# Kernel optimization log

Measured on AMD Instinct MI355X. Metric: run time of the kernel, lower is better.

Reference implementation:

```python
import jax, jax.numpy as jnp
import numpy as np

VOCAB, D, H = 32000, 256, 1024
B, S = 8, 4096
PAD = 0


def setup_inputs() -> dict:
    key = jax.random.key(0)
    ks = jax.random.split(key, 9)
    x = jax.random.randint(ks[0], (B, S), 0, VOCAB)
    emb = jax.random.normal(ks[1], (VOCAB, D), jnp.float32) * 0.02
    wq = jax.random.normal(ks[2], (D, D), jnp.float32) * 0.02
    wk = jax.random.normal(ks[3], (D, D), jnp.float32) * 0.02
    wv = jax.random.normal(ks[4], (D, D), jnp.float32) * 0.02
    w1 = jax.random.normal(ks[5], (H, D), jnp.float32) * 0.02
    b1 = jnp.zeros((H,), jnp.float32)
    w2 = jax.random.normal(ks[6], (VOCAB, H), jnp.float32) * 0.02
    b2 = jnp.zeros((VOCAB,), jnp.float32)
    return {"x": x, "emb": emb, "wq": wq, "wk": wk, "wv": wv,
            "w1": w1, "b1": b1, "w2": w2, "b2": b2}


def reference(x, emb, wq, wk, wv, w1, b1, w2, b2):
    # padding_idx=0: that embedding row is zero
    emb0 = emb.at[PAD].set(0.0)
    e = emb0[x]                                   # [B,S,D]
    keep = (x != PAD).astype(e.dtype)             # 1 where key is NOT masked
    q = jnp.einsum('bsd,ed->bse', e, wq)
    k = jnp.einsum('bsd,ed->bse', e, wk)
    v = jnp.einsum('bsd,ed->bse', e, wv)
    # Original: attn = q @ k^T, masked_fill padded keys -> 0, v_out = (attn @ v).sum(dim=1)
    # Reordered (identical math, O(S*D^2) instead of O(S^2)):
    #   v_out[b,:] = (sum_i q_i) @ (sum_j keep_j * k_j v_j^T)
    qsum = q.sum(axis=1)                          # [B,D]
    kv = jnp.einsum('bsd,bse->bde', k * keep[..., None], v)  # [B,D,D]
    v_out = jnp.einsum('bd,bde->be', qsum, kv)    # [B,D]
    h = jax.nn.relu(v_out @ w1.T + b1)            # [B,H]
    logits = h @ w2.T + b2                        # [B,VOCAB]
    return jax.nn.softmax(logits, axis=-1)
```

## Files before the change

kernel.cpp:

```cpp
#include <hip/hip_runtime.h>

#define BB 8
#define SS 4096
#define DD 256
#define HH 1024
#define VOCAB 32000
#define NCH 128
#define NLB 2000

typedef float v2f __attribute__((ext_vector_type(2)));


__global__ __launch_bounds__(256) void k_esum(const int* __restrict__ x,
        const float* __restrict__ emb, float* __restrict__ part_esum) {
    __shared__ int toks[32];
    const int b = blockIdx.y, chunk = blockIdx.x, tid = threadIdx.x;
    if (tid < 32) toks[tid] = x[b * SS + chunk * 32 + tid];
    __syncthreads();
    float a0 = 0.f, a1 = 0.f, a2 = 0.f, a3 = 0.f;
    for (int t = 0; t < 32; t += 4) {
        int t0 = toks[t], t1 = toks[t + 1], t2 = toks[t + 2], t3 = toks[t + 3];
        if (t0) a0 += emb[t0 * DD + tid];
        if (t1) a1 += emb[t1 * DD + tid];
        if (t2) a2 += emb[t2 * DD + tid];
        if (t3) a3 += emb[t3 * DD + tid];
    }
    part_esum[(b * NCH + chunk) * DD + tid] = (a0 + a1) + (a2 + a3);
}

__global__ __launch_bounds__(256) void k_qa(const float* __restrict__ part_esum,
        const float* __restrict__ wq, const float* __restrict__ wk,
        float* __restrict__ a) {
    const int b = blockIdx.x, tid = threadIdx.x, wid = tid >> 6, lane = tid & 63;
    __shared__ __align__(16) float es[DD];
    __shared__ __align__(16) float qs[DD];
    {
        float s0 = 0.f, s1 = 0.f, s2 = 0.f, s3 = 0.f;
        const float* p = part_esum + b * NCH * DD + tid;
        for (int c = 0; c < NCH; c += 4) {
            s0 += p[(c + 0) * DD]; s1 += p[(c + 1) * DD];
            s2 += p[(c + 2) * DD]; s3 += p[(c + 3) * DD];
        }
        es[tid] = (s0 + s1) + (s2 + s3);
    }
    __syncthreads();
    const float4 es4 = ((const float4*)es)[lane];
    for (int r0 = 0; r0 < 64; r0 += 4) {
        float dp[4];
        #pragma unroll
        for (int j = 0; j < 4; ++j) {
            const float4 w4 = ((const float4*)(wq + (wid * 64 + r0 + j) * DD))[lane];
            dp[j] = w4.x * es4.x + w4.y * es4.y + w4.z * es4.z + w4.w * es4.w;
        }
        #pragma unroll
        for (int off = 32; off; off >>= 1) {
            #pragma unroll
            for (int j = 0; j < 4; ++j) dp[j] += __shfl_xor(dp[j], off, 64);
        }
        if (lane < 4) qs[wid * 64 + r0 + lane] = dp[lane];
    }
    __syncthreads();
    float a0 = 0.f, a1 = 0.f, a2 = 0.f, a3 = 0.f;
    for (int e = 0; e < DD; e += 4) {
        a0 += wk[(e + 0) * DD + tid] * qs[e + 0];
        a1 += wk[(e + 1) * DD + tid] * qs[e + 1];
        a2 += wk[(e + 2) * DD + tid] * qs[e + 2];
        a3 += wk[(e + 3) * DD + tid] * qs[e + 3];
    }
    a[b * DD + tid] = (a0 + a1) + (a2 + a3);
}

__global__ __launch_bounds__(256) void k_u(const int* __restrict__ x,
        const float* __restrict__ emb, const float* __restrict__ a,
        float* __restrict__ part_u) {
    const int b = blockIdx.y, chunk = blockIdx.x, tid = threadIdx.x;
    const int wid = tid >> 6, lane = tid & 63;
    __shared__ int toks[32];
    __shared__ __align__(16) float ured[4][DD];
    if (tid < 32) toks[tid] = x[b * SS + chunk * 32 + tid];
    __syncthreads();
    const float4 a4 = ((const float4*)(a + b * DD))[lane];
    float4 up = {0.f, 0.f, 0.f, 0.f};
    #pragma unroll
    for (int tt = 0; tt < 32; tt += 16) {
        int tok[4]; float4 e4[4]; float dp[4];
        #pragma unroll
        for (int j = 0; j < 4; ++j) tok[j] = toks[tt + j * 4 + wid];
        #pragma unroll
        for (int j = 0; j < 4; ++j) {
            e4[j] = ((const float4*)(emb + tok[j] * DD))[lane];
            dp[j] = e4[j].x * a4.x + e4[j].y * a4.y + e4[j].z * a4.z + e4[j].w * a4.w;
        }
        #pragma unroll
        for (int off = 32; off; off >>= 1) {
            #pragma unroll
            for (int j = 0; j < 4; ++j) dp[j] += __shfl_xor(dp[j], off, 64);
        }
        #pragma unroll
        for (int j = 0; j < 4; ++j) {
            const float m = (tok[j] != 0) ? dp[j] : 0.f;
            up.x += m * e4[j].x; up.y += m * e4[j].y;
            up.z += m * e4[j].z; up.w += m * e4[j].w;
        }
    }
    ((float4*)ured[wid])[lane] = up;
    __syncthreads();
    part_u[(b * NCH + chunk) * DD + tid] =
        ured[0][tid] + ured[1][tid] + ured[2][tid] + ured[3][tid];
}

__global__ __launch_bounds__(256) void k_vout(const float* __restrict__ part_u,
        const float* __restrict__ wv, float* __restrict__ vout) {
    const int b = blockIdx.x, tid = threadIdx.x, wid = tid >> 6, lane = tid & 63;
    __shared__ __align__(16) float us[DD];
    {
        float s0 = 0.f, s1 = 0.f, s2 = 0.f, s3 = 0.f;
        const float* p = part_u + b * NCH * DD + tid;
        for (int c = 0; c < NCH; c += 4) {
            s0 += p[(c + 0) * DD]; s1 += p[(c + 1) * DD];
            s2 += p[(c + 2) * DD]; s3 += p[(c + 3) * DD];
        }
        us[tid] = (s0 + s1) + (s2 + s3);
    }
    __syncthreads();
    const float4 u4 = ((const float4*)us)[lane];
    for (int r0 = 0; r0 < 64; r0 += 4) {
        float dp[4];
        #pragma unroll
        for (int j = 0; j < 4; ++j) {
            const float4 w4 = ((const float4*)(wv + (wid * 64 + r0 + j) * DD))[lane];
            dp[j] = w4.x * u4.x + w4.y * u4.y + w4.z * u4.z + w4.w * u4.w;
        }
        #pragma unroll
        for (int off = 32; off; off >>= 1) {
            #pragma unroll
            for (int j = 0; j < 4; ++j) dp[j] += __shfl_xor(dp[j], off, 64);
        }
        if (lane < 4) vout[b * DD + wid * 64 + r0 + lane] = dp[lane];
    }
}

__global__ __launch_bounds__(256) void k_h(const float* __restrict__ vout,
        const float* __restrict__ w1, const float* __restrict__ b1,
        float* __restrict__ h) {
    const int b = blockIdx.y, tid = threadIdx.x, wid = tid >> 6, lane = tid & 63;
    const float4 v4 = ((const float4*)(vout + b * DD))[lane];
    const int rbase = blockIdx.x * 32 + wid * 8;
    float dp[8];
    #pragma unroll
    for (int r = 0; r < 8; ++r) {
        const float4 w4 = ((const float4*)(w1 + (rbase + r) * DD))[lane];
        dp[r] = w4.x * v4.x + w4.y * v4.y + w4.z * v4.z + w4.w * v4.w;
    }
    #pragma unroll
    for (int off = 32; off; off >>= 1) {
        #pragma unroll
        for (int r = 0; r < 8; ++r) dp[r] += __shfl_xor(dp[r], off, 64);
    }
    if (lane < 8) h[b * HH + rbase + lane] = fmaxf(dp[lane] + b1[rbase + lane], 0.f);
}

__global__ __launch_bounds__(256, 4) void k_logits(const float* __restrict__ h,
        const float* __restrict__ w2, const float* __restrict__ b2,
        float* __restrict__ out, float* __restrict__ spart) {
    const int tid = threadIdx.x, wid = tid >> 6, lane = tid & 63;
    const int half = lane >> 5;
    v2f hp[16];
    #pragma unroll
    for (int c = 0; c < 4; ++c) {
        const float4 ta = ((const float4*)(h + (2 * wid)     * HH + c * 256))[lane];
        const float4 tb = ((const float4*)(h + (2 * wid + 1) * HH + c * 256))[lane];
        hp[c * 4 + 0] = (v2f){ta.x, tb.x};
        hp[c * 4 + 1] = (v2f){ta.y, tb.y};
        hp[c * 4 + 2] = (v2f){ta.z, tb.z};
        hp[c * 4 + 3] = (v2f){ta.w, tb.w};
    }
    float m_run = -1e30f, s_run = 0.f;
    #pragma unroll 2
    for (int r = 0; r < 16; ++r) {
        const int i = blockIdx.x + r * NLB;
        const float4* row = (const float4*)(w2 + (size_t)i * HH);
        v2f acc = (v2f){0.f, 0.f};
        #pragma unroll
        for (int c = 0; c < 4; ++c) {
            const float4 w = row[c * 64 + lane];
            acc += hp[c * 4 + 0] * w.x;
            acc += hp[c * 4 + 1] * w.y;
            acc += hp[c * 4 + 2] * w.z;
            acc += hp[c * 4 + 3] * w.w;
        }
        const float send = (half == 0) ? acc.y : acc.x;
        const float keep = (half == 0) ? acc.x : acc.y;
        float s = keep + __shfl_xor(send, 32, 64);
        s += __shfl_xor(s, 16, 64);
        s += __shfl_xor(s, 8, 64);
        s += __shfl_xor(s, 4, 64);
        s += __shfl_xor(s, 2, 64);
        s += __shfl_xor(s, 1, 64);
        if ((lane & 31) == 0) {
            const float lg = s + b2[i];
            out[(2 * wid + half) * VOCAB + i] = lg;
            const float mn = fmaxf(m_run, lg);
            s_run = s_run * __expf(m_run - mn) + __expf(lg - mn);
            m_run = mn;
        }
    }
    if ((lane & 31) == 0)
        ((v2f*)spart)[(2 * wid + half) * NLB + blockIdx.x] = (v2f){m_run, s_run};
}

__global__ __launch_bounds__(256) void k_norm(const float* __restrict__ spart,
        float* __restrict__ out) {
    const int b = blockIdx.y, seg = blockIdx.x, tid = threadIdx.x;
    __shared__ float rm[256], rs[256];
    const v2f* p = (const v2f*)spart + b * NLB;
    float m = -1e30f, s = 0.f;
    for (int idx = tid; idx < NLB; idx += 256) {
        const v2f t = p[idx];
        const float mn = fmaxf(m, t.x);
        s = s * __expf(m - mn) + t.y * __expf(t.x - mn);
        m = mn;
    }
    rm[tid] = m; rs[tid] = s;
    __syncthreads();
    for (int st = 128; st; st >>= 1) {
        if (tid < st) {
            const float m2 = rm[tid + st], s2 = rs[tid + st];
            const float mn = fmaxf(rm[tid], m2);
            rs[tid] = rs[tid] * __expf(rm[tid] - mn) + s2 * __expf(m2 - mn);
            rm[tid] = mn;
        }
        __syncthreads();
    }
    const float gm = rm[0], ginv = 1.f / rs[0];
    float* lg = out + b * VOCAB + seg * 2000;
    for (int i = tid; i < 2000; i += 256) lg[i] = __expf(lg[i] - gm) * ginv;
}

extern "C" void kernel_launch(void* const* d_in, const int* in_sizes, int n_in,
                              void* d_out, int out_size, void* d_ws, size_t ws_size,
                              hipStream_t stream) {
    const int*   x   = (const int*)d_in[0];
    const float* emb = (const float*)d_in[1];
    const float* wq  = (const float*)d_in[2];
    const float* wk  = (const float*)d_in[3];
    const float* wv  = (const float*)d_in[4];
    const float* w1  = (const float*)d_in[5];
    const float* b1  = (const float*)d_in[6];
    const float* w2  = (const float*)d_in[7];
    const float* b2  = (const float*)d_in[8];
    float* out = (float*)d_out;
    float* ws  = (float*)d_ws;

    float* part_esum = ws;
    float* part_u    = ws + 262144;
    float* a         = ws + 524288;
    float* vout      = ws + 526336;
    float* h         = ws + 528384;
    float* spart     = ws + 536576;

    k_esum<<<dim3(NCH, BB), 256, 0, stream>>>(x, emb, part_esum);
    k_qa<<<BB, 256, 0, stream>>>(part_esum, wq, wk, a);
    k_u<<<dim3(NCH, BB), 256, 0, stream>>>(x, emb, a, part_u);
    k_vout<<<BB, 256, 0, stream>>>(part_u, wv, vout);
    k_h<<<dim3(32, BB), 256, 0, stream>>>(vout, w1, b1, h);
    k_logits<<<NLB, 256, 0, stream>>>(h, w2, b2, out, spart);
    k_norm<<<dim3(16, BB), 256, 0, stream>>>(spart, out);
}
```

Baseline: 88.24 us.

## Fuse reduction stages into producer kernels via last-block atomic counters

Merges the embedding-sum and q/a projection into one kernel, and merges the u accumulation, v_out projection and h MLP layer into another. Each merged kernel uses a per-batch atomic counter so that only the last finishing block does the follow-up reduction and small matvecs. This cuts the launch count from seven to five (plus a tiny counter-init kernel) and removes launch gaps between dependent stages. In exchange, the h layer is now computed by a single block per batch instead of 32 blocks, which serialises 1024 row dot-products onto one block.

```diff
diff --git a/kernel.cpp b/kernel.cpp
--- a/kernel.cpp
+++ b/kernel.cpp
@@ -11,29 +11,43 @@
 typedef float v2f __attribute__((ext_vector_type(2)));
 
 
-__global__ __launch_bounds__(256) void k_esum(const int* __restrict__ x,
-        const float* __restrict__ emb, float* __restrict__ part_esum) {
+__global__ void k_init(int* __restrict__ cnt) {
+    if (threadIdx.x < 16) cnt[threadIdx.x] = 0;
+}
+
+__global__ __launch_bounds__(256) void k1_esum_qa(const int* __restrict__ x,
+        const float* __restrict__ emb, const float* __restrict__ wq,
+        const float* __restrict__ wk, float* __restrict__ part_esum,
+        float* __restrict__ a, int* __restrict__ cnt) {
+    const int b = blockIdx.y, chunk = blockIdx.x, tid = threadIdx.x;
+    const int wid = tid >> 6, lane = tid & 63;
     __shared__ int toks[32];
-    const int b = blockIdx.y, chunk = blockIdx.x, tid = threadIdx.x;
-    if (tid < 32) toks[tid] = x[b * SS + chunk * 32 + tid];
-    __syncthreads();
-    float a0 = 0.f, a1 = 0.f, a2 = 0.f, a3 = 0.f;
-    for (int t = 0; t < 32; t += 4) {
-        int t0 = toks[t], t1 = toks[t + 1], t2 = toks[t + 2], t3 = toks[t + 3];
-        if (t0) a0 += emb[t0 * DD + tid];
-        if (t1) a1 += emb[t1 * DD + tid];
-        if (t2) a2 += emb[t2 * DD + tid];
-        if (t3) a3 += emb[t3 * DD + tid];
-    }
-    part_esum[(b * NCH + chunk) * DD + tid] = (a0 + a1) + (a2 + a3);
-}
-
-__global__ __launch_bounds__(256) void k_qa(const float* __restrict__ part_esum,
-        const float* __restrict__ wq, const float* __restrict__ wk,
-        float* __restrict__ a) {
-    const int b = blockIdx.x, tid = threadIdx.x, wid = tid >> 6, lane = tid & 63;
     __shared__ __align__(16) float es[DD];
     __shared__ __align__(16) float qs[DD];
+    __shared__ int is_last;
+
+    if (tid < 32) toks[tid] = x[b * SS + chunk * 32 + tid];
+    __syncthreads();
+    {
+        float a0 = 0.f, a1 = 0.f, a2 = 0.f, a3 = 0.f;
+        for (int t = 0; t < 32; t += 4) {
+            int t0 = toks[t], t1 = toks[t + 1], t2 = toks[t + 2], t3 = toks[t + 3];
+            if (t0) a0 += emb[t0 * DD + tid];
+            if (t1) a1 += emb[t1 * DD + tid];
+            if (t2) a2 += emb[t2 * DD + tid];
+            if (t3) a3 += emb[t3 * DD + tid];
+        }
+        part_esum[(b * NCH + chunk) * DD + tid] = (a0 + a1) + (a2 + a3);
+    }
+
+    if (tid == 0) {
+        __threadfence();
+        is_last = (atomicAdd(&cnt[b], 1) == NCH - 1);
+    }
+    __syncthreads();
+    if (!is_last) return;
+    __threadfence();
+
     {
         float s0 = 0.f, s1 = 0.f, s2 = 0.f, s3 = 0.f;
         const float* p = part_esum + b * NCH * DD + tid;
@@ -70,49 +84,60 @@
     a[b * DD + tid] = (a0 + a1) + (a2 + a3);
 }
 
-__global__ __launch_bounds__(256) void k_u(const int* __restrict__ x,
+__global__ __launch_bounds__(256) void k2_u_vout_h(const int* __restrict__ x,
         const float* __restrict__ emb, const float* __restrict__ a,
-        float* __restrict__ part_u) {
+        const float* __restrict__ wv, const float* __restrict__ w1,
+        const float* __restrict__ b1, float* __restrict__ part_u,
+        float* __restrict__ h, int* __restrict__ cnt) {
     const int b = blockIdx.y, chunk = blockIdx.x, tid = threadIdx.x;
     const int wid = tid >> 6, lane = tid & 63;
     __shared__ int toks[32];
     __shared__ __align__(16) float ured[4][DD];
+    __shared__ __align__(16) float us[DD];
+    __shared__ __align__(16) float vo[DD];
+    __shared__ int is_last;
+
     if (tid < 32) toks[tid] = x[b * SS + chunk * 32 + tid];
     __syncthreads();
-    const float4 a4 = ((const float4*)(a + b * DD))[lane];
-    float4 up = {0.f, 0.f, 0.f, 0.f};
-    #pragma unroll
-    for (int tt = 0; tt < 32; tt += 16) {
-        int tok[4]; float4 e4[4]; float dp[4];
-        #pragma unroll
-        for (int j = 0; j < 4; ++j) tok[j] = toks[tt + j * 4 + wid];
-        #pragma unroll
-        for (int j = 0; j < 4; ++j) {
-            e4[j] = ((const float4*)(emb + tok[j] * DD))[lane];
-            dp[j] = e4[j].x * a4.x + e4[j].y * a4.y + e4[j].z * a4.z + e4[j].w * a4.w;
-        }
-        #pragma unroll
-        for (int off = 32; off; off >>= 1) {
-            #pragma unroll
-            for (int j = 0; j < 4; ++j) dp[j] += __shfl_xor(dp[j], off, 64);
-        }
-        #pragma unroll
-        for (int j = 0; j < 4; ++j) {
-            const float m = (tok[j] != 0) ? dp[j] : 0.f;
-            up.x += m * e4[j].x; up.y += m * e4[j].y;
-            up.z += m * e4[j].z; up.w += m * e4[j].w;
-        }
-    }
-    ((float4*)ured[wid])[lane] = up;
-    __syncthreads();
-    part_u[(b * NCH + chunk) * DD + tid] =
-        ured[0][tid] + ured[1][tid] + ured[2][tid] + ured[3][tid];
-}
-
-__global__ __launch_bounds__(256) void k_vout(const float* __restrict__ part_u,
-        const float* __restrict__ wv, float* __restrict__ vout) {
-    const int b = blockIdx.x, tid = threadIdx.x, wid = tid >> 6, lane = tid & 63;
-    __shared__ __align__(16) float us[DD];
+    {
+        const float4 a4 = ((const float4*)(a + b * DD))[lane];
+        float4 up = {0.f, 0.f, 0.f, 0.f};
+        #pragma unroll
+        for (int tt = 0; tt < 32; tt += 16) {
+            int tok[4]; float4 e4[4]; float dp[4];
+            #pragma unroll
+            for (int j = 0; j < 4; ++j) tok[j] = toks[tt + j * 4 + wid];
+            #pragma unroll
+            for (int j = 0; j < 4; ++j) {
+                e4[j] = ((const float4*)(emb + tok[j] * DD))[lane];
+                dp[j] = e4[j].x * a4.x + e4[j].y * a4.y + e4[j].z * a4.z + e4[j].w * a4.w;
+            }
+            #pragma unroll
+            for (int off = 32; off; off >>= 1) {
+                #pragma unroll
+                for (int j = 0; j < 4; ++j) dp[j] += __shfl_xor(dp[j], off, 64);
+            }
+            #pragma unroll
+            for (int j = 0; j < 4; ++j) {
+                const float m = (tok[j] != 0) ? dp[j] : 0.f;
+                up.x += m * e4[j].x; up.y += m * e4[j].y;
+                up.z += m * e4[j].z; up.w += m * e4[j].w;
+            }
+        }
+        ((float4*)ured[wid])[lane] = up;
+        __syncthreads();
+        part_u[(b * NCH + chunk) * DD + tid] =
+            ured[0][tid] + ured[1][tid] + ured[2][tid] + ured[3][tid];
+    }
+
+    if (tid == 0) {
+        __threadfence();
+        is_last = (atomicAdd(&cnt[8 + b], 1) == NCH - 1);
+    }
+    __syncthreads();
+    if (!is_last) return;
+    __threadfence();
+
     {
         float s0 = 0.f, s1 = 0.f, s2 = 0.f, s3 = 0.f;
         const float* p = part_u + b * NCH * DD + tid;
@@ -123,41 +148,42 @@
         us[tid] = (s0 + s1) + (s2 + s3);
     }
     __syncthreads();
-    const float4 u4 = ((const float4*)us)[lane];
-    for (int r0 = 0; r0 < 64; r0 += 4) {
-        float dp[4];
-        #pragma unroll
-        for (int j = 0; j < 4; ++j) {
-            const float4 w4 = ((const float4*)(wv + (wid * 64 + r0 + j) * DD))[lane];
-            dp[j] = w4.x * u4.x + w4.y * u4.y + w4.z * u4.z + w4.w * u4.w;
-        }
-        #pragma unroll
-        for (int off = 32; off; off >>= 1) {
-            #pragma unroll
-            for (int j = 0; j < 4; ++j) dp[j] += __shfl_xor(dp[j], off, 64);
-        }
-        if (lane < 4) vout[b * DD + wid * 64 + r0 + lane] = dp[lane];
-    }
-}
-
-__global__ __launch_bounds__(256) void k_h(const float* __restrict__ vout,
-        const float* __restrict__ w1, const float* __restrict__ b1,
-        float* __restrict__ h) {
-    const int b = blockIdx.y, tid = threadIdx.x, wid = tid >> 6, lane = tid & 63;
-    const float4 v4 = ((const float4*)(vout + b * DD))[lane];
-    const int rbase = blockIdx.x * 32 + wid * 8;
-    float dp[8];
-    #pragma unroll
-    for (int r = 0; r < 8; ++r) {
-        const float4 w4 = ((const float4*)(w1 + (rbase + r) * DD))[lane];
-        dp[r] = w4.x * v4.x + w4.y * v4.y + w4.z * v4.z + w4.w * v4.w;
-    }
-    #pragma unroll
-    for (int off = 32; off; off >>= 1) {
-        #pragma unroll
-        for (int r = 0; r < 8; ++r) dp[r] += __shfl_xor(dp[r], off, 64);
-    }
-    if (lane < 8) h[b * HH + rbase + lane] = fmaxf(dp[lane] + b1[rbase + lane], 0.f);
+    {
+        const float4 u4 = ((const float4*)us)[lane];
+        for (int r0 = 0; r0 < 64; r0 += 4) {
+            float dp[4];
+            #pragma unroll
+            for (int j = 0; j < 4; ++j) {
+                const float4 w4 = ((const float4*)(wv + (wid * 64 + r0 + j) * DD))[lane];
+                dp[j] = w4.x * u4.x + w4.y * u4.y + w4.z * u4.z + w4.w * u4.w;
+            }
+            #pragma unroll
+            for (int off = 32; off; off >>= 1) {
+                #pragma unroll
+                for (int j = 0; j < 4; ++j) dp[j] += __shfl_xor(dp[j], off, 64);
+            }
+            if (lane < 4) vo[wid * 64 + r0 + lane] = dp[lane];
+        }
+    }
+    __syncthreads();
+    {
+        const float4 v4 = ((const float4*)vo)[lane];
+        for (int r0 = 0; r0 < 256; r0 += 4) {
+            const int rb = wid * 256 + r0;
+            float dp[4];
+            #pragma unroll
+            for (int j = 0; j < 4; ++j) {
+                const float4 w4 = ((const float4*)(w1 + (rb + j) * DD))[lane];
+                dp[j] = w4.x * v4.x + w4.y * v4.y + w4.z * v4.z + w4.w * v4.w;
+            }
+            #pragma unroll
+            for (int off = 32; off; off >>= 1) {
+                #pragma unroll
+                for (int j = 0; j < 4; ++j) dp[j] += __shfl_xor(dp[j], off, 64);
+            }
+            if (lane < 4) h[b * HH + rb + lane] = fmaxf(dp[lane] + b1[rb + lane], 0.f);
+        }
+    }
 }
 
 __global__ __launch_bounds__(256, 4) void k_logits(const float* __restrict__ h,
@@ -255,15 +281,13 @@
     float* part_esum = ws;
     float* part_u    = ws + 262144;
     float* a         = ws + 524288;
-    float* vout      = ws + 526336;
-    float* h         = ws + 528384;
-    float* spart     = ws + 536576;
-
-    k_esum<<<dim3(NCH, BB), 256, 0, stream>>>(x, emb, part_esum);
-    k_qa<<<BB, 256, 0, stream>>>(part_esum, wq, wk, a);
-    k_u<<<dim3(NCH, BB), 256, 0, stream>>>(x, emb, a, part_u);
-    k_vout<<<BB, 256, 0, stream>>>(part_u, wv, vout);
-    k_h<<<dim3(32, BB), 256, 0, stream>>>(vout, w1, b1, h);
+    float* h         = ws + 526336;
+    float* spart     = ws + 534528;
+    int*   cnt       = (int*)(ws + 566528);
+
+    k_init<<<1, 64, 0, stream>>>(cnt);
+    k1_esum_qa<<<dim3(NCH, BB), 256, 0, stream>>>(x, emb, wq, wk, part_esum, a, cnt);
+    k2_u_vout_h<<<dim3(NCH, BB), 256, 0, stream>>>(x, emb, a, wv, w1, b1, part_u, h, cnt);
     k_logits<<<NLB, 256, 0, stream>>>(h, w2, b2, out, spart);
     k_norm<<<dim3(16, BB), 256, 0, stream>>>(spart, out);
 }
```

Result: slower. 188.1 us (+113.2%).
